# Performance work log

Measured on AMD Instinct MI355X. Metric: run time of the kernel, lower is better.

## Reference

```python
import jax, jax.numpy as jnp
import numpy as np

HIDDEN = 1024
HEADS = 16
HEAD_DIM = HIDDEN // HEADS


def setup_inputs() -> dict:
    key = jax.random.key(0)
    k1, k2, k3, k4 = jax.random.split(key, 4)
    x = jax.random.normal(k1, (4, 2048, HIDDEN), dtype=jnp.float32)
    # qkv: Linear(hidden, 3*hidden, bias=False) -> weight [3*hidden, hidden]
    w_qkv = jax.random.normal(k2, (3 * HIDDEN, HIDDEN), dtype=jnp.float32) * (HIDDEN ** -0.5)
    # out_proj: Linear(hidden, hidden) with bias
    w_out = jax.random.normal(k3, (HIDDEN, HIDDEN), dtype=jnp.float32) * (HIDDEN ** -0.5)
    b_out = jax.random.normal(k4, (HIDDEN,), dtype=jnp.float32) * 0.01
    return {"x": x, "w_qkv": w_qkv, "w_out": w_out, "b_out": b_out}


def reference(x, w_qkv, w_out, b_out):
    B, N, _ = x.shape
    scale = HEAD_DIM ** -0.5
    qkv = jnp.einsum('bnc,dc->bnd', x, w_qkv)            # [B,N,3*hidden]
    qkv = qkv.reshape(B, N, 3, HEADS, HEAD_DIM)
    qkv = jnp.transpose(qkv, (2, 0, 3, 1, 4))            # [3,B,H,N,hd]
    q, k, v = qkv[0], qkv[1], qkv[2]
    att = jnp.einsum('bhxd,bhyd->bhxy', q, k) * scale    # [B,H,N,N]
    att = jax.nn.softmax(att, axis=-1)
    out = jnp.einsum('bhxy,bhyd->bhxd', att, v)          # [B,H,N,hd]
    out = jnp.transpose(out, (0, 2, 1, 3)).reshape(B, N, HIDDEN)
    out = jnp.einsum('bnc,dc->bnd', out, w_out) + b_out
    return out
```

## Files before the change

kernel.cpp:

```cpp
#include <hip/hip_runtime.h>

typedef unsigned short u16;
typedef short short8 __attribute__((ext_vector_type(8)));
typedef float f32x4 __attribute__((ext_vector_type(4)));
typedef float f32x16 __attribute__((ext_vector_type(16)));
typedef unsigned short u16x4 __attribute__((ext_vector_type(4)));
typedef unsigned int u32x4 __attribute__((ext_vector_type(4)));

#define MFMA16(a, b, c) __builtin_amdgcn_mfma_f32_16x16x32_bf16((a), (b), (c), 0, 0, 0)
#define MFMA32(a, b, c) __builtin_amdgcn_mfma_f32_32x32x16_bf16((a), (b), (c), 0, 0, 0)

#if __has_builtin(__builtin_amdgcn_exp2f)
#define EXP2F(x) __builtin_amdgcn_exp2f(x)
#else
#define EXP2F(x) exp2f(x)
#endif

__device__ __forceinline__ u16 f2bf(float f) {
    unsigned u = __builtin_bit_cast(unsigned, f);
    u += 0x7FFFu + ((u >> 16) & 1u);
    return (u16)(u >> 16);
}

__device__ __forceinline__ void async16(void* lds, const void* g) {
    __builtin_amdgcn_global_load_lds(
        (const __attribute__((address_space(1))) void*)g,
        (__attribute__((address_space(3))) void*)lds, 16, 0, 0);
}

__device__ __forceinline__ unsigned cvtpk(float lo, float hi) {
    unsigned r;
    asm("v_cvt_pk_bf16_f32 %0, %1, %2" : "=v"(r) : "v"(lo), "v"(hi));
    return r;
}
__device__ __forceinline__ void plswap(unsigned& a, unsigned& b) {
    asm("v_permlane32_swap_b32 %0, %1" : "+v"(a), "+v"(b));
}

__device__ __forceinline__ void packP(const f32x16& s, short8& f0, short8& f1) {
    u32x4 u0, u1;
    {
        unsigned a = cvtpk(s[0], s[1]), b = cvtpk(s[4], s[5]);
        plswap(a, b);
        unsigned c = cvtpk(s[2], s[3]), d = cvtpk(s[6], s[7]);
        plswap(c, d);
        u0[0] = a; u0[1] = c; u0[2] = b; u0[3] = d;
    }
    {
        unsigned a = cvtpk(s[8], s[9]), b = cvtpk(s[12], s[13]);
        plswap(a, b);
        unsigned c = cvtpk(s[10], s[11]), d = cvtpk(s[14], s[15]);
        plswap(c, d);
        u1[0] = a; u1[1] = c; u1[2] = b; u1[3] = d;
    }
    f0 = __builtin_bit_cast(short8, u0);
    f1 = __builtin_bit_cast(short8, u1);
}

__global__ __launch_bounds__(256) void cast3(const float* __restrict__ x,
                                             const float* __restrict__ wqkv,
                                             const float* __restrict__ wout,
                                             u16* __restrict__ dst) {
    const int blk = blockIdx.x;
    const float* src;
    int idx;
    float sc = 1.0f;
    u16* out;
    if (blk < 8192) {
        src = x; out = dst; idx = (blk * 256 + threadIdx.x) * 4;
    } else if (blk < 11264) {
        src = wqkv; out = dst + (size_t)8192 * 1024;
        idx = ((blk - 8192) * 256 + threadIdx.x) * 4;
        if (idx < 1024 * 1024) sc = 0.18033688011112042f;
    } else {
        src = wout; out = dst + (size_t)11264 * 1024;
        idx = ((blk - 11264) * 256 + threadIdx.x) * 4;
    }
    float4 v = *(const float4*)(src + idx);
    u16x4 r;
    r[0] = f2bf(v.x * sc); r[1] = f2bf(v.y * sc);
    r[2] = f2bf(v.z * sc); r[3] = f2bf(v.w * sc);
    *(u16x4*)(out + idx) = r;
}

__global__ __launch_bounds__(512, 2) void gemm256(const u16* __restrict__ A,
                                                  const u16* __restrict__ B,
                                                  u16* __restrict__ qk,
                                                  u16* __restrict__ vt) {
    __shared__ u16 lds[2][2][16384];
    const int tid = threadIdx.x;
    const int l = tid & 63;
    const int w = tid >> 6;
    const int g = l >> 4, lo = l & 15;
    const int wrow = w >> 2, wcol = w & 3;
    const int tm = blockIdx.x & 31, tn = blockIdx.x >> 5;
    const int rowBase = tm << 8, colBase = tn << 8;

    const int srow = tid >> 3;
    const int scol = (((tid * 16) ^ (((tid >> 3) & 7) << 4)) & 127) >> 1;
    const u16* pa = A + (size_t)(rowBase + srow) * 1024 + scol;
    const u16* pb = B + (size_t)(colBase + srow) * 1024 + scol;
    const int ldsOff = tid * 16;

    int abase[2], bbase[2];
#pragma unroll
    for (int k = 0; k < 2; ++k) {
        abase[k] = (((wrow * 128 + lo) * 128 + k * 64 + g * 16) ^ ((lo & 7) << 4));
        bbase[k] = (((wcol * 64 + lo) * 128 + k * 64 + g * 16) ^ ((lo & 7) << 4));
    }

    f32x4 acc[8][4] = {};

#define STAGE256(buf, kt)                                                                   \
    {                                                                                       \
        const u16* sa = pa + (kt) * 64;                                                     \
        const u16* sb = pb + (kt) * 64;                                                     \
        _Pragma("unroll")                                                                   \
        for (int i = 0; i < 4; ++i) {                                                       \
            async16((char*)lds[buf][0] + ldsOff + i * 8192, sa + (size_t)i * 64 * 1024);    \
            async16((char*)lds[buf][1] + ldsOff + i * 8192, sb + (size_t)i * 64 * 1024);    \
        }                                                                                   \
    }

    STAGE256(0, 0);
    __syncthreads();

    for (int kt = 0; kt < 16; ++kt) {
        const int cur = kt & 1;
        if (kt < 15) STAGE256(cur ^ 1, kt + 1);
        const char* la = (const char*)lds[cur][0];
        const char* lb = (const char*)lds[cur][1];

        short8 bf[4][2], af[4][2];
#pragma unroll
        for (int n = 0; n < 4; ++n)
#pragma unroll
            for (int k = 0; k < 2; ++k)
                bf[n][k] = *(const short8*)(lb + bbase[k] + n * 2048);
#pragma unroll
        for (int m = 0; m < 4; ++m)
#pragma unroll
            for (int k = 0; k < 2; ++k)
                af[m][k] = *(const short8*)(la + abase[k] + m * 2048);
        __builtin_amdgcn_s_setprio(1);
#pragma unroll
        for (int m = 0; m < 4; ++m)
#pragma unroll
            for (int n = 0; n < 4; ++n) {
                acc[m][n] = MFMA16(af[m][0], bf[n][0], acc[m][n]);
                acc[m][n] = MFMA16(af[m][1], bf[n][1], acc[m][n]);
            }
        __builtin_amdgcn_s_setprio(0);
#pragma unroll
        for (int m = 0; m < 4; ++m)
#pragma unroll
            for (int k = 0; k < 2; ++k)
                af[m][k] = *(const short8*)(la + abase[k] + (m + 4) * 2048);
        __builtin_amdgcn_s_setprio(1);
#pragma unroll
        for (int m = 0; m < 4; ++m)
#pragma unroll
            for (int n = 0; n < 4; ++n) {
                acc[m + 4][n] = MFMA16(af[m][0], bf[n][0], acc[m + 4][n]);
                acc[m + 4][n] = MFMA16(af[m][1], bf[n][1], acc[m + 4][n]);
            }
        __builtin_amdgcn_s_setprio(0);
        __syncthreads();
    }
#undef STAGE256

    if (colBase < 2048) {
#pragma unroll
        for (int n = 0; n < 4; ++n) {
            const int c = colBase + wcol * 64 + n * 16 + lo;
#pragma unroll
            for (int m = 0; m < 8; ++m) {
                const int r0 = rowBase + wrow * 128 + m * 16 + g * 4;
#pragma unroll
                for (int i = 0; i < 4; ++i)
                    qk[(size_t)(r0 + i) * 2048 + c] = f2bf(acc[m][n][i]);
            }
        }
    } else {
        const int b = rowBase >> 11;
#pragma unroll
        for (int n = 0; n < 4; ++n) {
            const int c = colBase + wcol * 64 + n * 16 + lo;
            const int hh = (c - 2048) >> 6, d = (c - 2048) & 63;
            u16* vrow = vt + ((size_t)((b * 16 + hh) * 64 + d)) * 2048;
#pragma unroll
            for (int m = 0; m < 8; ++m) {
                const int r0 = rowBase + wrow * 128 + m * 16 + g * 4;
                u16x4 pk;
#pragma unroll
                for (int i = 0; i < 4; ++i) pk[i] = f2bf(acc[m][n][i]);
                *(u16x4*)(vrow + (r0 & 2047)) = pk;
            }
        }
    }
}

__global__ __launch_bounds__(256, 2) void gemm_bt(const u16* __restrict__ A,
                                                  const u16* __restrict__ B,
                                                  float* __restrict__ Cf,
                                                  const float* __restrict__ bias,
                                                  int M, int N, int K) {
    __shared__ u16 As[128 * 32];
    __shared__ u16 Bs[128 * 32];
    const int tid = threadIdx.x;
    const int w = tid >> 6, l = tid & 63;
    const int g = l >> 4, lo = l & 15;
    const int mtiles = M >> 7;
    const int tm = blockIdx.x % mtiles, tn = blockIdx.x / mtiles;
    const int rowBase = tm << 7, colBase = tn << 7;
    const int wrow = w >> 1, wcol = w & 1;

    f32x4 acc[4][4] = {};

    const int srow = l >> 2;
    const int scol = (l & 3) * 8;
    const int nk = K >> 5;
    for (int kt = 0; kt < nk; ++kt) {
        const int kbase = kt * 32 + scol;
#pragma unroll
        for (int it = 0; it < 2; ++it) {
            const int seg = it * 4 + w;
            const int r = seg * 16 + srow;
            async16(&As[seg * 512], &A[(size_t)(rowBase + r) * K + kbase]);
            async16(&Bs[seg * 512], &B[(size_t)(colBase + r) * K + kbase]);
        }
        __syncthreads();
        short8 af[4], bf[4];
#pragma unroll
        for (int mi = 0; mi < 4; ++mi)
            af[mi] = *(const short8*)&As[(wrow * 64 + mi * 16 + lo) * 32 + g * 8];
#pragma unroll
        for (int ni = 0; ni < 4; ++ni)
            bf[ni] = *(const short8*)&Bs[(wcol * 64 + ni * 16 + lo) * 32 + g * 8];
#pragma unroll
        for (int mi = 0; mi < 4; ++mi)
#pragma unroll
            for (int ni = 0; ni < 4; ++ni)
                acc[mi][ni] = MFMA16(af[mi], bf[ni], acc[mi][ni]);
        __syncthreads();
    }

#pragma unroll
    for (int ni = 0; ni < 4; ++ni) {
        const int c = colBase + wcol * 64 + ni * 16 + lo;
        const float bv = bias[c];
#pragma unroll
        for (int mi = 0; mi < 4; ++mi) {
            const int r0 = rowBase + wrow * 64 + mi * 16 + g * 4;
#pragma unroll
            for (int i = 0; i < 4; ++i)
                Cf[(size_t)(r0 + i) * N + c] = acc[mi][ni][i] + bv;
        }
    }
}

__global__ __launch_bounds__(256, 4) void attn_fwd(const u16* __restrict__ qkb,
                                                   const u16* __restrict__ vtg,
                                                   u16* __restrict__ outb) {
    __shared__ u16 Ks[2][64 * 64];
    __shared__ u16 Vs[2][64 * 64];
    const int tid = threadIdx.x;
    const int w = tid >> 6, l = tid & 63;
    const int hi = l >> 5, lq = l & 31;

    const int lin = (blockIdx.x & 7) * 128 + (blockIdx.x >> 3);
    const int bh = lin >> 4, qt = lin & 15;
    const int b = bh >> 4, h = bh & 15;
    const size_t rowQ = (size_t)b * 2048 + qt * 128 + w * 32;

    short8 qf[4];
#pragma unroll
    for (int ks = 0; ks < 4; ++ks)
        qf[ks] = *(const short8*)(qkb + (rowQ + lq) * 2048 + h * 64 + ks * 16 + hi * 8);

    int koff[4];
#pragma unroll
    for (int ks = 0; ks < 4; ++ks)
        koff[ks] = (lq * 128 + ks * 32 + hi * 16) ^ ((lq & 7) << 4);

    const int L0 = tid * 16, L1 = tid * 16 + 4096;
    const int kr0 = L0 >> 7, kc0 = ((L0 ^ ((kr0 & 7) << 4)) & 127) >> 1;
    const int kr1 = L1 >> 7, kc1 = ((L1 ^ ((kr1 & 7) << 4)) & 127) >> 1;
    const u16* ks0 = qkb + (size_t)(b * 2048 + kr0) * 2048 + 1024 + h * 64 + kc0;
    const u16* ks1 = qkb + (size_t)(b * 2048 + kr1) * 2048 + 1024 + h * 64 + kc1;
    const u16* vs0 = vtg + ((size_t)bh * 64 + kr0) * 2048 + kc0;
    const u16* vs1 = vtg + ((size_t)bh * 64 + kr1) * 2048 + kc1;
    const size_t KADV = (size_t)64 * 2048;

    f32x16 O0, O1, Ol;
#pragma unroll
    for (int i = 0; i < 16; ++i) { O0[i] = 0.f; O1[i] = 0.f; Ol[i] = 0.f; }
    const f32x16 Z = {};
    const short8 onesv = {16256, 16256, 16256, 16256, 16256, 16256, 16256, 16256};

    async16((char*)Ks[0] + L0, ks0); async16((char*)Ks[0] + L1, ks1);
    async16((char*)Vs[0] + L0, vs0); async16((char*)Vs[0] + L1, vs1);
    ks0 += KADV; ks1 += KADV; vs0 += 64; vs1 += 64;

    int cur = 0;
    for (int kt = 0; kt < 32; ++kt) {
        __syncthreads();
        if (kt < 31) {
            const int nx = cur ^ 1;
            async16((char*)Ks[nx] + L0, ks0); async16((char*)Ks[nx] + L1, ks1);
            async16((char*)Vs[nx] + L0, vs0); async16((char*)Vs[nx] + L1, vs1);
            ks0 += KADV; ks1 += KADV; vs0 += 64; vs1 += 64;
        }
        const char* kb = (const char*)Ks[cur];
        const char* vb = (const char*)Vs[cur];

#pragma unroll
        for (int t = 0; t < 2; ++t) {
            const int tb = t * 4096;
            __builtin_amdgcn_s_setprio(1);
            f32x16 s = MFMA32(*(const short8*)(kb + koff[0] + tb), qf[0], Z);
            s = MFMA32(*(const short8*)(kb + koff[1] + tb), qf[1], s);
            s = MFMA32(*(const short8*)(kb + koff[2] + tb), qf[2], s);
            s = MFMA32(*(const short8*)(kb + koff[3] + tb), qf[3], s);
            __builtin_amdgcn_s_setprio(0);

#pragma unroll
            for (int i = 0; i < 16; ++i) s[i] = EXP2F(s[i]);

            short8 p0, p1;
            packP(s, p0, p1);

            __builtin_amdgcn_s_setprio(1);
            Ol = MFMA32(p0, onesv, Ol);
            Ol = MFMA32(p1, onesv, Ol);
            O0 = MFMA32(p0, *(const short8*)(vb + koff[t * 2]), O0);
            O1 = MFMA32(p0, *(const short8*)(vb + koff[t * 2] + 4096), O1);
            O0 = MFMA32(p1, *(const short8*)(vb + koff[t * 2 + 1]), O0);
            O1 = MFMA32(p1, *(const short8*)(vb + koff[t * 2 + 1] + 4096), O1);
            __builtin_amdgcn_s_setprio(0);
        }
        cur ^= 1;
    }

#pragma unroll
    for (int r = 0; r < 16; ++r) {
        const int qrow = (r & 3) + 8 * (r >> 2) + 4 * hi;
        const float linv = 1.0f / Ol[r];
        u16* op = outb + (rowQ + qrow) * 1024 + h * 64 + lq;
        op[0] = f2bf(O0[r] * linv);
        op[32] = f2bf(O1[r] * linv);
    }
}

extern "C" void kernel_launch(void* const* d_in, const int* in_sizes, int n_in,
                              void* d_out, int out_size, void* d_ws, size_t ws_size,
                              hipStream_t stream) {
    const float* x     = (const float*)d_in[0];
    const float* w_qkv = (const float*)d_in[1];
    const float* w_out = (const float*)d_in[2];
    const float* b_out = (const float*)d_in[3];
    float* out = (float*)d_out;

    u16* xb    = (u16*)d_ws;
    u16* wqkvb = xb    + (size_t)8192 * 1024;
    u16* woutb = wqkvb + (size_t)3072 * 1024;
    u16* qkb   = woutb + (size_t)1024 * 1024;
    u16* vtg   = qkb   + (size_t)8192 * 2048;
    u16* attb  = vtg   + (size_t)64 * 64 * 2048;

    cast3<<<12288, 256, 0, stream>>>(x, w_qkv, w_out, xb);

    gemm256<<<384, 512, 0, stream>>>(xb, wqkvb, qkb, vtg);

    attn_fwd<<<1024, 256, 0, stream>>>(qkb, vtg, attb);

    gemm_bt<<<dim3((8192 / 128) * (1024 / 128)), 256, 0, stream>>>(
        attb, woutb, out, b_out, 8192, 1024, 1024);
}
```

Before: 187.0 us.

## Split V projection into separate 128-tile GEMM with transposed store

The fused QKV GEMM launch is split in two. The large 256-tile kernel now computes only Q and K, with 256 blocks. A new 128x128-tile kernel computes V and writes it transposed for the attention kernel. This is intended to even out wave quantization across CUs and to simplify the epilogue branch. The cost is an extra launch and a less optimized, single-buffered GEMM for the V portion.

```diff
diff --git a/kernel.cpp b/kernel.cpp
--- a/kernel.cpp
+++ b/kernel.cpp
@@ -85,8 +85,7 @@
 
 __global__ __launch_bounds__(512, 2) void gemm256(const u16* __restrict__ A,
                                                   const u16* __restrict__ B,
-                                                  u16* __restrict__ qk,
-                                                  u16* __restrict__ vt) {
+                                                  u16* __restrict__ qk) {
     __shared__ u16 lds[2][2][16384];
     const int tid = threadIdx.x;
     const int l = tid & 63;
@@ -169,33 +168,73 @@
     }
 #undef STAGE256
 
-    if (colBase < 2048) {
-#pragma unroll
-        for (int n = 0; n < 4; ++n) {
-            const int c = colBase + wcol * 64 + n * 16 + lo;
-#pragma unroll
-            for (int m = 0; m < 8; ++m) {
-                const int r0 = rowBase + wrow * 128 + m * 16 + g * 4;
-#pragma unroll
-                for (int i = 0; i < 4; ++i)
-                    qk[(size_t)(r0 + i) * 2048 + c] = f2bf(acc[m][n][i]);
-            }
-        }
-    } else {
-        const int b = rowBase >> 11;
-#pragma unroll
-        for (int n = 0; n < 4; ++n) {
-            const int c = colBase + wcol * 64 + n * 16 + lo;
-            const int hh = (c - 2048) >> 6, d = (c - 2048) & 63;
-            u16* vrow = vt + ((size_t)((b * 16 + hh) * 64 + d)) * 2048;
-#pragma unroll
-            for (int m = 0; m < 8; ++m) {
-                const int r0 = rowBase + wrow * 128 + m * 16 + g * 4;
-                u16x4 pk;
-#pragma unroll
-                for (int i = 0; i < 4; ++i) pk[i] = f2bf(acc[m][n][i]);
-                *(u16x4*)(vrow + (r0 & 2047)) = pk;
-            }
+#pragma unroll
+    for (int n = 0; n < 4; ++n) {
+        const int c = colBase + wcol * 64 + n * 16 + lo;
+#pragma unroll
+        for (int m = 0; m < 8; ++m) {
+            const int r0 = rowBase + wrow * 128 + m * 16 + g * 4;
+#pragma unroll
+            for (int i = 0; i < 4; ++i)
+                qk[(size_t)(r0 + i) * 2048 + c] = f2bf(acc[m][n][i]);
+        }
+    }
+}
+
+__global__ __launch_bounds__(256, 2) void gemmV(const u16* __restrict__ A,
+                                                const u16* __restrict__ Bv,
+                                                u16* __restrict__ vt) {
+    __shared__ u16 As[128 * 32];
+    __shared__ u16 Bs[128 * 32];
+    const int tid = threadIdx.x;
+    const int w = tid >> 6, l = tid & 63;
+    const int g = l >> 4, lo = l & 15;
+    const int tm = blockIdx.x & 63, tn = blockIdx.x >> 6;
+    const int rowBase = tm << 7, colBase = tn << 7;
+    const int wrow = w >> 1, wcol = w & 1;
+
+    f32x4 acc[4][4] = {};
+
+    const int srow = l >> 2;
+    const int scol = (l & 3) * 8;
+    for (int kt = 0; kt < 32; ++kt) {
+        const int kbase = kt * 32 + scol;
+#pragma unroll
+        for (int it = 0; it < 2; ++it) {
+            const int seg = it * 4 + w;
+            const int r = seg * 16 + srow;
+            async16(&As[seg * 512], &A[(size_t)(rowBase + r) * 1024 + kbase]);
+            async16(&Bs[seg * 512], &Bv[(size_t)(colBase + r) * 1024 + kbase]);
+        }
+        __syncthreads();
+        short8 af[4], bf[4];
+#pragma unroll
+        for (int mi = 0; mi < 4; ++mi)
+            af[mi] = *(const short8*)&As[(wrow * 64 + mi * 16 + lo) * 32 + g * 8];
+#pragma unroll
+        for (int ni = 0; ni < 4; ++ni)
+            bf[ni] = *(const short8*)&Bs[(wcol * 64 + ni * 16 + lo) * 32 + g * 8];
+#pragma unroll
+        for (int mi = 0; mi < 4; ++mi)
+#pragma unroll
+            for (int ni = 0; ni < 4; ++ni)
+                acc[mi][ni] = MFMA16(af[mi], bf[ni], acc[mi][ni]);
+        __syncthreads();
+    }
+
+    const int b = rowBase >> 11;
+#pragma unroll
+    for (int ni = 0; ni < 4; ++ni) {
+        const int c = colBase + wcol * 64 + ni * 16 + lo;
+        const int hh = c >> 6, d = c & 63;
+        u16* vrow = vt + ((size_t)((b * 16 + hh) * 64 + d)) * 2048;
+#pragma unroll
+        for (int mi = 0; mi < 4; ++mi) {
+            const int r0 = rowBase + wrow * 64 + mi * 16 + g * 4;
+            u16x4 pk;
+#pragma unroll
+            for (int i = 0; i < 4; ++i) pk[i] = f2bf(acc[mi][ni][i]);
+            *(u16x4*)(vrow + (r0 & 2047)) = pk;
         }
     }
 }
@@ -370,7 +409,8 @@
 
     cast3<<<12288, 256, 0, stream>>>(x, w_qkv, w_out, xb);
 
-    gemm256<<<384, 512, 0, stream>>>(xb, wqkvb, qkb, vtg);
+    gemm256<<<256, 512, 0, stream>>>(xb, wqkvb, qkb);
+    gemmV<<<512, 256, 0, stream>>>(xb, wqkvb + (size_t)2048 * 1024, vtg);
 
     attn_fwd<<<1024, 256, 0, stream>>>(qkb, vtg, attb);
 
```

New measurement: 187.5 us. Within noise of the previous version (+0.2%).
